# Optimization experiments

Hardware: AMD Instinct MI355X
Metric: run time of the kernel (lower is better)

Reference implementation:

```python
import jax, jax.numpy as jnp
import numpy as np

N = 20000      # atoms
E = 320000     # pairs (avg degree 16)
F = 64         # per-atom features
NRBF = 32      # radial basis functions
RC = 1.0       # maximum_interaction_radius


def _decompose(t):
    # X = I + A + S (irreducible decomposition of 3x3 tensors)
    diag_mean = jnp.diagonal(t, axis1=-2, axis2=-1).mean(-1)
    I = diag_mean[..., None, None] * jnp.eye(3, dtype=t.dtype)
    A = 0.5 * (t - jnp.swapaxes(t, -1, -2))
    S = 0.5 * (t + jnp.swapaxes(t, -1, -2)) - I
    return I, A, S


def _tnorm(t):
    # Frobenius norm^2 over the trailing 3x3 -> [N, F]
    return (t ** 2).sum((-2, -1))


def _lin_t(t, W):
    # channel-mixing linear on the feature axis of [N, F, 3, 3]
    return jnp.einsum('nfij,gf->ngij', t, W)


def setup_inputs():
    key = jax.random.key(0)
    ks = jax.random.split(key, 14)
    inp = {
        'X': jax.random.normal(ks[0], (N, F, 3, 3), jnp.float32) * 0.1,
        'pair_indices': jax.random.randint(ks[1], (2, E), 0, N, jnp.int32),
        'd_ij': jax.random.uniform(ks[2], (E, 1), jnp.float32),
        'radial_feature_vector': jax.random.normal(ks[3], (E, NRBF), jnp.float32),
        'atomic_charges': jax.random.normal(ks[4], (N,), jnp.float32) * 0.1,
        # mlp_scalar: NRBF -> F -> 2F -> 3F (Dense = Linear + activation)
        'W0': jax.random.normal(ks[5], (F, NRBF), jnp.float32) / np.sqrt(NRBF),
        'b0': jnp.zeros((F,), jnp.float32),
        'W1': jax.random.normal(ks[6], (2 * F, F), jnp.float32) / np.sqrt(F),
        'b1': jnp.zeros((2 * F,), jnp.float32),
        'W2': jax.random.normal(ks[7], (3 * F, 2 * F), jnp.float32) / np.sqrt(2 * F),
        'b2': jnp.zeros((3 * F,), jnp.float32),
        # 6 bias-free FxF tensor linears
        'Wt': jax.random.normal(ks[8], (6, F, F), jnp.float32) / np.sqrt(F),
    }
    return inp


def reference(X, pair_indices, d_ij, radial_feature_vector, atomic_charges,
              W0, b0, W1, b1, W2, b2, Wt):
    silu = jax.nn.silu
    n_atoms = X.shape[0]
    src = pair_indices[1]  # gathered
    dst = pair_indices[0]  # scattered (index_add_)

    # cosine cutoff, [E, 1]
    C = (0.5 * (jnp.cos(jnp.pi * d_ij / RC) + 1.0)
         * (d_ij < RC).astype(X.dtype)).reshape(-1, 1)

    h = silu(radial_feature_vector @ W0.T + b0)
    h = silu(h @ W1.T + b1)
    h = silu(h @ W2.T + b2)                 # [E, 3F]
    rfv = (h * C).reshape(-1, F, 3)          # [E, F, 3]

    X = X / (_tnorm(X) + 1.0)[..., None, None]
    I, A, S = _decompose(X)
    I = _lin_t(I, Wt[0])
    A = _lin_t(A, Wt[1])
    S = _lin_t(S, Wt[2])
    Y = I + A + S

    def mp(r, T):
        # gather-mul-scatter: [E,F,3,3] messages reduced to [N,F,3,3]
        msg = r[:, :, None, None] * T[src]
        return jax.ops.segment_sum(msg, dst, num_segments=n_atoms)

    msg = mp(rfv[..., 0], I) + mp(rfv[..., 1], A) + mp(rfv[..., 2], S)

    # O(3) group
    q = (1.0 + 0.1 * atomic_charges)[:, None, None, None]
    I, A, S = _decompose(q * (jnp.matmul(msg, Y) + jnp.matmul(Y, msg)))

    normp1 = (_tnorm(I + A + S) + 1.0)[..., None, None]
    I, A, S = I / normp1, A / normp1, S / normp1
    I = _lin_t(I, Wt[3])
    A = _lin_t(A, Wt[4])
    S = _lin_t(S, Wt[5])
    dX = I + A + S

    X = X + dX + q * jnp.matmul(dX, dX)
    return X
```

## Files before the change

kernel.cpp:

```cpp
#include <hip/hip_runtime.h>
#include <hip/hip_bf16.h>
#include <cmath>

#define N_ATOMS 20000
#define NE      320000
#define FDIM    64
#define NRBF    32
#define PI_F    3.14159265358979323846f

typedef __attribute__((ext_vector_type(8))) short bf16x8;
typedef __attribute__((ext_vector_type(4))) float f32x4;
typedef __attribute__((ext_vector_type(4))) _Float16 f16x4;

#define MFMA16(a, b, c) __builtin_amdgcn_mfma_f32_16x16x32_bf16(a, b, c, 0, 0, 0)

__device__ __forceinline__ float silu(float x) {
    return x * __builtin_amdgcn_rcpf(1.0f + __expf(-x));
}

__device__ __forceinline__ unsigned short f2bf_rne(float x) {
    unsigned u = __float_as_uint(x);
    u += 0x7fffu + ((u >> 16) & 1u);
    return (unsigned short)(u >> 16);
}

__device__ __forceinline__ void split8(const float* v, bf16x8& hi, bf16x8& lo) {
#pragma unroll
    for (int j = 0; j < 8; j++) {
        unsigned u = __float_as_uint(v[j]);
        float hf = __uint_as_float(u & 0xffff0000u);
        hi[j] = (short)(u >> 16);
        lo[j] = (short)f2bf_rne(v[j] - hf);
    }
}

__global__ void prep_kernel(const float* __restrict__ Wt, float* __restrict__ wtT,
                            const float* __restrict__ W0, const float* __restrict__ W1,
                            const float* __restrict__ W2,
                            unsigned short* __restrict__ f0h, unsigned short* __restrict__ f0l,
                            unsigned short* __restrict__ f1h, unsigned short* __restrict__ f1l,
                            unsigned short* __restrict__ f2h, unsigned short* __restrict__ f2l,
                            const int* __restrict__ dst, int* __restrict__ deg) {
    int idx = blockIdx.x * 256 + threadIdx.x;
    if (idx < 24576) {
        int k = idx >> 12;
        int r = idx & 4095;
        int g = r >> 6;
        int f = r & 63;
        wtT[k * 4096 + f * 64 + g] = Wt[idx];
    } else if (idx < 59392) {
        int t = idx - 24576;
        const float* W;
        unsigned short *fh, *fl;
        int K, NT;
        if (t < 2048)       { W = W0; fh = f0h; fl = f0l;             K = 32;  NT = 4; }
        else if (t < 10240) { W = W1; fh = f1h; fl = f1l; t -= 2048;  K = 64;  NT = 8; }
        else                { W = W2; fh = f2h; fl = f2l; t -= 10240; K = 128; NT = 12; }
        int j = t & 7;
        int lane = (t >> 3) & 63;
        int rest = t >> 9;
        int nt = rest % NT;
        int ks = rest / NT;
        int k = ks * 32 + ((lane >> 4) & 3) * 8 + j;
        int n = nt * 16 + (lane & 15);
        float w = W[n * K + k];
        unsigned u = __float_as_uint(w);
        float hf = __uint_as_float(u & 0xffff0000u);
        fh[t] = (unsigned short)(u >> 16);
        fl[t] = f2bf_rne(w - hf);
    } else if (idx < 59392 + NE) {
        int e = idx - 59392;
        atomicAdd(&deg[dst[e]], 1);
    }
}

__global__ void scan_kernel(const int* __restrict__ deg, int* __restrict__ off) {
    __shared__ int part[1024];
    int t = threadIdx.x;
    const int CH = (N_ATOMS + 1023) / 1024;
    int base = t * CH;
    int s = 0;
    for (int i = 0; i < CH; i++) {
        int idx = base + i;
        if (idx < N_ATOMS) s += deg[idx];
    }
    part[t] = s;
    __syncthreads();
    for (int ofs = 1; ofs < 1024; ofs <<= 1) {
        int v = (t >= ofs) ? part[t - ofs] : 0;
        __syncthreads();
        part[t] += v;
        __syncthreads();
    }
    int run = (t == 0) ? 0 : part[t - 1];
    for (int i = 0; i < CH; i++) {
        int idx = base + i;
        if (idx < N_ATOMS) {
            off[idx] = run;
            run += deg[idx];
        }
    }
    if (t == 1023) off[N_ATOMS] = run;
}

__global__ void fill_kernel(const int* __restrict__ dst, const int* __restrict__ srcArr,
                            const int* __restrict__ off, int* __restrict__ cursor,
                            int* __restrict__ sbkt, int* __restrict__ slotOf) {
    int e = blockIdx.x * 256 + threadIdx.x;
    if (e >= NE) return;
    int d = dst[e];
    int pos = atomicAdd(&cursor[d], 1);
    int slot = off[d] + pos;
    sbkt[slot] = srcArr[e];
    slotOf[e] = slot;
}

#define H1S 68
#define H2S 132
__global__ __launch_bounds__(128) void mlp_mfma_kernel(
    const float* __restrict__ rfv, const float* __restrict__ dij,
    const float* __restrict__ b0, const float* __restrict__ b1, const float* __restrict__ b2,
    const unsigned short* __restrict__ f0h, const unsigned short* __restrict__ f0l,
    const unsigned short* __restrict__ f1h, const unsigned short* __restrict__ f1l,
    const unsigned short* __restrict__ f2h, const unsigned short* __restrict__ f2l,
    const int* __restrict__ slotOf,
    __hip_bfloat16* __restrict__ r) {
    __shared__ float h1s[2][32][H1S];
    __shared__ float h2s[2][32][H2S];
    const int w = threadIdx.x >> 6;
    const int lane = threadIdx.x & 63;
    const int q = lane >> 4;
    const int c = lane & 15;
    const int e0 = (blockIdx.x * 2 + w) * 32;
    float (*h1)[H1S] = h1s[w];
    float (*h2)[H2S] = h2s[w];

    {
        bf16x8 ah[2], al[2];
#pragma unroll
        for (int mt = 0; mt < 2; mt++) {
            float v[8];
            const float* p = rfv + (size_t)(e0 + mt * 16 + c) * 32 + q * 8;
            *(float4*)(v)     = *(const float4*)(p);
            *(float4*)(v + 4) = *(const float4*)(p + 4);
            split8(v, ah[mt], al[mt]);
        }
#pragma unroll
        for (int nt = 0; nt < 4; nt++) {
            float bias = b0[nt * 16 + c];
            f32x4 acc[2];
            acc[0] = {bias, bias, bias, bias};
            acc[1] = acc[0];
            bf16x8 bh = *(const bf16x8*)(f0h + (size_t)(nt * 64 + lane) * 8);
            bf16x8 bl = *(const bf16x8*)(f0l + (size_t)(nt * 64 + lane) * 8);
#pragma unroll
            for (int mt = 0; mt < 2; mt++) {
                acc[mt] = MFMA16(al[mt], bh, acc[mt]);
                acc[mt] = MFMA16(ah[mt], bl, acc[mt]);
                acc[mt] = MFMA16(ah[mt], bh, acc[mt]);
            }
#pragma unroll
            for (int mt = 0; mt < 2; mt++)
#pragma unroll
                for (int reg = 0; reg < 4; reg++)
                    h1[mt * 16 + q * 4 + reg][nt * 16 + c] = silu(acc[mt][reg]);
        }
    }

    {
        bf16x8 ah[2][2], al[2][2];
#pragma unroll
        for (int mt = 0; mt < 2; mt++)
#pragma unroll
            for (int ks = 0; ks < 2; ks++) {
                float v[8];
                const float* p = &h1[mt * 16 + c][ks * 32 + q * 8];
                *(float4*)(v)     = *(const float4*)(p);
                *(float4*)(v + 4) = *(const float4*)(p + 4);
                split8(v, ah[mt][ks], al[mt][ks]);
            }
#pragma unroll
        for (int nt = 0; nt < 8; nt++) {
            float bias = b1[nt * 16 + c];
            f32x4 acc[2];
            acc[0] = {bias, bias, bias, bias};
            acc[1] = acc[0];
#pragma unroll
            for (int ks = 0; ks < 2; ks++) {
                bf16x8 bh = *(const bf16x8*)(f1h + (size_t)((ks * 8 + nt) * 64 + lane) * 8);
                bf16x8 bl = *(const bf16x8*)(f1l + (size_t)((ks * 8 + nt) * 64 + lane) * 8);
#pragma unroll
                for (int mt = 0; mt < 2; mt++) {
                    acc[mt] = MFMA16(al[mt][ks], bh, acc[mt]);
                    acc[mt] = MFMA16(ah[mt][ks], bl, acc[mt]);
                    acc[mt] = MFMA16(ah[mt][ks], bh, acc[mt]);
                }
            }
#pragma unroll
            for (int mt = 0; mt < 2; mt++)
#pragma unroll
                for (int reg = 0; reg < 4; reg++)
                    h2[mt * 16 + q * 4 + reg][nt * 16 + c] = silu(acc[mt][reg]);
        }
    }

    {
        bf16x8 ah[2][4], al[2][4];
#pragma unroll
        for (int mt = 0; mt < 2; mt++)
#pragma unroll
            for (int ks = 0; ks < 4; ks++) {
                float v[8];
                const float* p = &h2[mt * 16 + c][ks * 32 + q * 8];
                *(float4*)(v)     = *(const float4*)(p);
                *(float4*)(v + 4) = *(const float4*)(p + 4);
                split8(v, ah[mt][ks], al[mt][ks]);
            }
        float cut[2][4];
        int srow[2][4];
#pragma unroll
        for (int mt = 0; mt < 2; mt++)
#pragma unroll
            for (int reg = 0; reg < 4; reg++) {
                int e = e0 + mt * 16 + q * 4 + reg;
                float d = dij[e];
                cut[mt][reg] = (d < 1.0f) ? 0.5f * (__cosf(PI_F * d) + 1.0f) : 0.0f;
                srow[mt][reg] = slotOf[e];
            }
#pragma unroll
        for (int nt = 0; nt < 12; nt++) {
            float bias = b2[nt * 16 + c];
            f32x4 acc[2];
            acc[0] = {bias, bias, bias, bias};
            acc[1] = acc[0];
#pragma unroll
            for (int ks = 0; ks < 4; ks++) {
                bf16x8 bh = *(const bf16x8*)(f2h + (size_t)((ks * 12 + nt) * 64 + lane) * 8);
                bf16x8 bl = *(const bf16x8*)(f2l + (size_t)((ks * 12 + nt) * 64 + lane) * 8);
#pragma unroll
                for (int mt = 0; mt < 2; mt++) {
                    acc[mt] = MFMA16(al[mt][ks], bh, acc[mt]);
                    acc[mt] = MFMA16(ah[mt][ks], bl, acc[mt]);
                    acc[mt] = MFMA16(ah[mt][ks], bh, acc[mt]);
                }
            }
#pragma unroll
            for (int mt = 0; mt < 2; mt++)
#pragma unroll
                for (int reg = 0; reg < 4; reg++)
                    r[(size_t)srow[mt][reg] * 192 + nt * 16 + c] =
                        __float2bfloat16(silu(acc[mt][reg]) * cut[mt][reg]);
        }
    }
}

__global__ __launch_bounds__(256) void lin1_kernel(
    const float* __restrict__ X, const float* __restrict__ wtT,
    _Float16* __restrict__ comp, float* __restrict__ Yb) {
    __shared__ float lds[4][64 * 11];
    int w = threadIdx.x >> 6;
    int l = threadIdx.x & 63;
    int a = blockIdx.x * 4 + w;

    {
        const float* x = X + ((size_t)a * 64 + l) * 9;
        float v[9];
#pragma unroll
        for (int i = 0; i < 9; i++) v[i] = x[i];
        float t2 = 0.f;
#pragma unroll
        for (int i = 0; i < 9; i++) t2 += v[i] * v[i];
        float inv = 1.0f / (t2 + 1.0f);
#pragma unroll
        for (int i = 0; i < 9; i++) v[i] *= inv;
        float iso = (v[0] + v[4] + v[8]) * (1.0f / 3.0f);
        float* o = &lds[w][l * 11];
        o[0] = iso;
        o[1] = 0.5f * (v[1] - v[3]);
        o[2] = 0.5f * (v[2] - v[6]);
        o[3] = 0.5f * (v[5] - v[7]);
        o[4] = v[0] - iso;
        o[5] = 0.5f * (v[1] + v[3]);
        o[6] = 0.5f * (v[2] + v[6]);
        o[7] = v[4] - iso;
        o[8] = 0.5f * (v[5] + v[7]);
        o[9] = v[8] - iso;
    }
    __syncthreads();
    {
        int g = l;
        const float* w0 = wtT;
        const float* w1 = wtT + 4096;
        const float* w2 = wtT + 8192;
        float acc[10];
#pragma unroll
        for (int c = 0; c < 10; c++) acc[c] = 0.f;
        for (int f = 0; f < 64; f++) {
            float wI = w0[f * 64 + g];
            float wA = w1[f * 64 + g];
            float wS = w2[f * 64 + g];
            const float* rf = &lds[w][f * 11];
            acc[0] += wI * rf[0];
            acc[1] += wA * rf[1];
            acc[2] += wA * rf[2];
            acc[3] += wA * rf[3];
#pragma unroll
            for (int c = 4; c < 10; c++) acc[c] += wS * rf[c];
        }
        _Float16* co = comp + ((size_t)a * 64 + g) * 12;
        f16x4 c0 = {(_Float16)acc[0], (_Float16)acc[1], (_Float16)acc[2], (_Float16)acc[3]};
        f16x4 c1 = {(_Float16)acc[4], (_Float16)acc[5], (_Float16)acc[6], (_Float16)acc[7]};
        f16x4 c2 = {(_Float16)acc[8], (_Float16)acc[9], (_Float16)0.f, (_Float16)0.f};
        *(f16x4*)(co)     = c0;
        *(f16x4*)(co + 4) = c1;
        *(f16x4*)(co + 8) = c2;
        float* y = Yb + ((size_t)a * 64 + g) * 9;
        y[0] = acc[0] + acc[4];
        y[1] = acc[5] + acc[1];
        y[2] = acc[6] + acc[2];
        y[3] = acc[5] - acc[1];
        y[4] = acc[0] + acc[7];
        y[5] = acc[8] + acc[3];
        y[6] = acc[6] - acc[2];
        y[7] = acc[8] - acc[3];
        y[8] = acc[0] + acc[9];
    }
}

__global__ __launch_bounds__(256) void msg_lin2_kernel(
    const int* __restrict__ off, const int* __restrict__ sbkt,
    const __hip_bfloat16* __restrict__ r,
    const _Float16* __restrict__ comp, const float* __restrict__ Yb,
    const float* __restrict__ X, const float* __restrict__ charges,
    const float* __restrict__ wtT, float* __restrict__ out) {
    __shared__ float lds[4][64 * 11];
    int w = threadIdx.x >> 6;
    int l = threadIdx.x & 63;
    int a = blockIdx.x * 4 + w;
    float q = 1.0f + 0.1f * charges[a];

    float m[10];
#pragma unroll
    for (int c = 0; c < 10; c++) m[c] = 0.f;
    {
        int beg = off[a], end = off[a + 1];
        if (beg < end) {
            __hip_bfloat16 ra, rb, rc;
            f16x4 c0, c1, c2;
            {
                const __hip_bfloat16* rp = r + (size_t)beg * 192 + l * 3;
                ra = rp[0]; rb = rp[1]; rc = rp[2];
                const _Float16* cp = comp + ((size_t)sbkt[beg] * 64 + l) * 12;
                c0 = *(const f16x4*)(cp);
                c1 = *(const f16x4*)(cp + 4);
                c2 = *(const f16x4*)(cp + 8);
            }
            for (int i = beg + 1; i < end; i++) {
                const __hip_bfloat16* rp = r + (size_t)i * 192 + l * 3;
                __hip_bfloat16 na = rp[0], nb = rp[1], nc = rp[2];
                const _Float16* cp = comp + ((size_t)sbkt[i] * 64 + l) * 12;
                f16x4 n0 = *(const f16x4*)(cp);
                f16x4 n1 = *(const f16x4*)(cp + 4);
                f16x4 n2 = *(const f16x4*)(cp + 8);
                float r0 = __bfloat162float(ra);
                float r1 = __bfloat162float(rb);
                float r2 = __bfloat162float(rc);
                m[0] += r0 * (float)c0[0];
                m[1] += r1 * (float)c0[1];
                m[2] += r1 * (float)c0[2];
                m[3] += r1 * (float)c0[3];
                m[4] += r2 * (float)c1[0];
                m[5] += r2 * (float)c1[1];
                m[6] += r2 * (float)c1[2];
                m[7] += r2 * (float)c1[3];
                m[8] += r2 * (float)c2[0];
                m[9] += r2 * (float)c2[1];
                ra = na; rb = nb; rc = nc;
                c0 = n0; c1 = n1; c2 = n2;
            }
            float r0 = __bfloat162float(ra);
            float r1 = __bfloat162float(rb);
            float r2 = __bfloat162float(rc);
            m[0] += r0 * (float)c0[0];
            m[1] += r1 * (float)c0[1];
            m[2] += r1 * (float)c0[2];
            m[3] += r1 * (float)c0[3];
            m[4] += r2 * (float)c1[0];
            m[5] += r2 * (float)c1[1];
            m[6] += r2 * (float)c1[2];
            m[7] += r2 * (float)c1[3];
            m[8] += r2 * (float)c2[0];
            m[9] += r2 * (float)c2[1];
        }
    }

    {
        float M[9];
        M[0] = m[0] + m[4]; M[1] = m[5] + m[1]; M[2] = m[6] + m[2];
        M[3] = m[5] - m[1]; M[4] = m[0] + m[7]; M[5] = m[8] + m[3];
        M[6] = m[6] - m[2]; M[7] = m[8] - m[3]; M[8] = m[0] + m[9];
        const float* yp = Yb + ((size_t)a * 64 + l) * 9;
        float Y[9];
#pragma unroll
        for (int i = 0; i < 9; i++) Y[i] = yp[i];
        float P[9];
#pragma unroll
        for (int i = 0; i < 3; i++) {
#pragma unroll
            for (int j = 0; j < 3; j++) {
                float s = 0.f;
#pragma unroll
                for (int k = 0; k < 3; k++)
                    s += M[i * 3 + k] * Y[k * 3 + j] + Y[i * 3 + k] * M[k * 3 + j];
                P[i * 3 + j] = q * s;
            }
        }
        float t2 = 0.f;
#pragma unroll
        for (int i = 0; i < 9; i++) t2 += P[i] * P[i];
        float inv = 1.0f / (t2 + 1.0f);
        float iso = (P[0] + P[4] + P[8]) * (1.0f / 3.0f);
        float* o = &lds[w][l * 11];
        o[0] = iso * inv;
        o[1] = 0.5f * (P[1] - P[3]) * inv;
        o[2] = 0.5f * (P[2] - P[6]) * inv;
        o[3] = 0.5f * (P[5] - P[7]) * inv;
        o[4] = (P[0] - iso) * inv;
        o[5] = 0.5f * (P[1] + P[3]) * inv;
        o[6] = 0.5f * (P[2] + P[6]) * inv;
        o[7] = (P[4] - iso) * inv;
        o[8] = 0.5f * (P[5] + P[7]) * inv;
        o[9] = (P[8] - iso) * inv;
    }
    __syncthreads();
    {
        int g = l;
        const float* w3 = wtT + 3 * 4096;
        const float* w4 = wtT + 4 * 4096;
        const float* w5 = wtT + 5 * 4096;
        float acc[10];
#pragma unroll
        for (int c = 0; c < 10; c++) acc[c] = 0.f;
        for (int f = 0; f < 64; f++) {
            float wI = w3[f * 64 + g];
            float wA = w4[f * 64 + g];
            float wS = w5[f * 64 + g];
            const float* rf = &lds[w][f * 11];
            acc[0] += wI * rf[0];
            acc[1] += wA * rf[1];
            acc[2] += wA * rf[2];
            acc[3] += wA * rf[3];
#pragma unroll
            for (int c = 4; c < 10; c++) acc[c] += wS * rf[c];
        }
        float D[9];
        D[0] = acc[0] + acc[4]; D[1] = acc[5] + acc[1]; D[2] = acc[6] + acc[2];
        D[3] = acc[5] - acc[1]; D[4] = acc[0] + acc[7]; D[5] = acc[8] + acc[3];
        D[6] = acc[6] - acc[2]; D[7] = acc[8] - acc[3]; D[8] = acc[0] + acc[9];

        const float* x = X + ((size_t)a * 64 + g) * 9;
        float xv[9];
#pragma unroll
        for (int i = 0; i < 9; i++) xv[i] = x[i];
        float t2 = 0.f;
#pragma unroll
        for (int i = 0; i < 9; i++) t2 += xv[i] * xv[i];
        float invn = 1.0f / (t2 + 1.0f);
#pragma unroll
        for (int i = 0; i < 9; i++) xv[i] *= invn;

        float DD[9];
#pragma unroll
        for (int i = 0; i < 3; i++) {
#pragma unroll
            for (int j = 0; j < 3; j++) {
                float s = 0.f;
#pragma unroll
                for (int k = 0; k < 3; k++) s += D[i * 3 + k] * D[k * 3 + j];
                DD[i * 3 + j] = s;
            }
        }
        float* op = out + ((size_t)a * 64 + g) * 9;
#pragma unroll
        for (int i = 0; i < 9; i++) op[i] = xv[i] + D[i] + q * DD[i];
    }
}

extern "C" void kernel_launch(void* const* d_in, const int* in_sizes, int n_in,
                              void* d_out, int out_size, void* d_ws, size_t ws_size,
                              hipStream_t stream) {
    const float* X       = (const float*)d_in[0];
    const int*   pair    = (const int*)d_in[1];
    const float* dij     = (const float*)d_in[2];
    const float* rfv     = (const float*)d_in[3];
    const float* charges = (const float*)d_in[4];
    const float* W0      = (const float*)d_in[5];
    const float* b0      = (const float*)d_in[6];
    const float* W1      = (const float*)d_in[7];
    const float* b1      = (const float*)d_in[8];
    const float* W2      = (const float*)d_in[9];
    const float* b2      = (const float*)d_in[10];
    const float* Wt      = (const float*)d_in[11];
    float* out = (float*)d_out;

    const int* dst = pair;
    const int* src = pair + NE;

    char* ws = (char*)d_ws;
    size_t ofs = 0;
    auto alloc = [&](size_t bytes) {
        void* p = ws + ofs;
        ofs += (bytes + 255) & ~(size_t)255;
        return p;
    };
    float* wtT  = (float*)alloc((size_t)6 * 4096 * 4);
    unsigned short* f0h = (unsigned short*)alloc(2048 * 2);
    unsigned short* f0l = (unsigned short*)alloc(2048 * 2);
    unsigned short* f1h = (unsigned short*)alloc(8192 * 2);
    unsigned short* f1l = (unsigned short*)alloc(8192 * 2);
    unsigned short* f2h = (unsigned short*)alloc(24576 * 2);
    unsigned short* f2l = (unsigned short*)alloc(24576 * 2);
    _Float16* comp = (_Float16*)alloc((size_t)N_ATOMS * FDIM * 12 * 2);
    __hip_bfloat16* rbuf = (__hip_bfloat16*)alloc((size_t)NE * 192 * 2);
    int* deg    = (int*)alloc((size_t)N_ATOMS * 4);
    int* offarr = (int*)alloc((size_t)(N_ATOMS + 1) * 4);
    int* cursor = (int*)alloc((size_t)N_ATOMS * 4);
    int* sbkt   = (int*)alloc((size_t)NE * 4);
    int* slotOf = (int*)alloc((size_t)NE * 4);
    float* Yb   = out;

    hipMemsetAsync(deg, 0, (size_t)N_ATOMS * 4, stream);
    hipMemsetAsync(cursor, 0, (size_t)N_ATOMS * 4, stream);

    prep_kernel<<<(59392 + NE + 255) / 256, 256, 0, stream>>>(
        Wt, wtT, W0, W1, W2, f0h, f0l, f1h, f1l, f2h, f2l, dst, deg);
    scan_kernel<<<1, 1024, 0, stream>>>(deg, offarr);
    fill_kernel<<<NE / 256, 256, 0, stream>>>(dst, src, offarr, cursor, sbkt, slotOf);

    mlp_mfma_kernel<<<NE / 64, 128, 0, stream>>>(
        rfv, dij, b0, b1, b2, f0h, f0l, f1h, f1l, f2h, f2l, slotOf, rbuf);

    lin1_kernel<<<N_ATOMS / 4, 256, 0, stream>>>(X, wtT, comp, Yb);

    msg_lin2_kernel<<<N_ATOMS / 4, 256, 0, stream>>>(
        offarr, sbkt, rbuf, comp, Yb, X, charges, wtT, out);
}
```

Baseline: 460.2 us.

## Fuse lin1 into MLP kernel and store radial weights in planar layout

```diff
diff --git a/kernel.cpp b/kernel.cpp
--- a/kernel.cpp
+++ b/kernel.cpp
@@ -117,14 +117,15 @@
 
 #define H1S 68
 #define H2S 132
-__global__ __launch_bounds__(128) void mlp_mfma_kernel(
+__global__ __launch_bounds__(128) void mlp_lin1_kernel(
     const float* __restrict__ rfv, const float* __restrict__ dij,
     const float* __restrict__ b0, const float* __restrict__ b1, const float* __restrict__ b2,
     const unsigned short* __restrict__ f0h, const unsigned short* __restrict__ f0l,
     const unsigned short* __restrict__ f1h, const unsigned short* __restrict__ f1l,
     const unsigned short* __restrict__ f2h, const unsigned short* __restrict__ f2l,
-    const int* __restrict__ slotOf,
-    __hip_bfloat16* __restrict__ r) {
+    const int* __restrict__ slotOf, __hip_bfloat16* __restrict__ r,
+    const float* __restrict__ X, const float* __restrict__ wtT,
+    _Float16* __restrict__ comp, float* __restrict__ Yb) {
     __shared__ float h1s[2][32][H1S];
     __shared__ float h2s[2][32][H2S];
     const int w = threadIdx.x >> 6;
@@ -244,86 +245,88 @@
                     acc[mt] = MFMA16(ah[mt][ks], bh, acc[mt]);
                 }
             }
+            int k = nt * 16 + c;
+            int ld = k / 3;
+            int jm = k - ld * 3;
+            int co = jm * 64 + ld;
 #pragma unroll
             for (int mt = 0; mt < 2; mt++)
 #pragma unroll
                 for (int reg = 0; reg < 4; reg++)
-                    r[(size_t)srow[mt][reg] * 192 + nt * 16 + c] =
+                    r[(size_t)srow[mt][reg] * 192 + co] =
                         __float2bfloat16(silu(acc[mt][reg]) * cut[mt][reg]);
         }
     }
-}
-
-__global__ __launch_bounds__(256) void lin1_kernel(
-    const float* __restrict__ X, const float* __restrict__ wtT,
-    _Float16* __restrict__ comp, float* __restrict__ Yb) {
-    __shared__ float lds[4][64 * 11];
-    int w = threadIdx.x >> 6;
-    int l = threadIdx.x & 63;
-    int a = blockIdx.x * 4 + w;
-
-    {
-        const float* x = X + ((size_t)a * 64 + l) * 9;
-        float v[9];
-#pragma unroll
-        for (int i = 0; i < 9; i++) v[i] = x[i];
-        float t2 = 0.f;
-#pragma unroll
-        for (int i = 0; i < 9; i++) t2 += v[i] * v[i];
-        float inv = 1.0f / (t2 + 1.0f);
-#pragma unroll
-        for (int i = 0; i < 9; i++) v[i] *= inv;
-        float iso = (v[0] + v[4] + v[8]) * (1.0f / 3.0f);
-        float* o = &lds[w][l * 11];
-        o[0] = iso;
-        o[1] = 0.5f * (v[1] - v[3]);
-        o[2] = 0.5f * (v[2] - v[6]);
-        o[3] = 0.5f * (v[5] - v[7]);
-        o[4] = v[0] - iso;
-        o[5] = 0.5f * (v[1] + v[3]);
-        o[6] = 0.5f * (v[2] + v[6]);
-        o[7] = v[4] - iso;
-        o[8] = 0.5f * (v[5] + v[7]);
-        o[9] = v[8] - iso;
-    }
-    __syncthreads();
-    {
-        int g = l;
-        const float* w0 = wtT;
-        const float* w1 = wtT + 4096;
-        const float* w2 = wtT + 8192;
-        float acc[10];
-#pragma unroll
-        for (int c = 0; c < 10; c++) acc[c] = 0.f;
-        for (int f = 0; f < 64; f++) {
-            float wI = w0[f * 64 + g];
-            float wA = w1[f * 64 + g];
-            float wS = w2[f * 64 + g];
-            const float* rf = &lds[w][f * 11];
-            acc[0] += wI * rf[0];
-            acc[1] += wA * rf[1];
-            acc[2] += wA * rf[2];
-            acc[3] += wA * rf[3];
-#pragma unroll
-            for (int c = 4; c < 10; c++) acc[c] += wS * rf[c];
-        }
-        _Float16* co = comp + ((size_t)a * 64 + g) * 12;
-        f16x4 c0 = {(_Float16)acc[0], (_Float16)acc[1], (_Float16)acc[2], (_Float16)acc[3]};
-        f16x4 c1 = {(_Float16)acc[4], (_Float16)acc[5], (_Float16)acc[6], (_Float16)acc[7]};
-        f16x4 c2 = {(_Float16)acc[8], (_Float16)acc[9], (_Float16)0.f, (_Float16)0.f};
-        *(f16x4*)(co)     = c0;
-        *(f16x4*)(co + 4) = c1;
-        *(f16x4*)(co + 8) = c2;
-        float* y = Yb + ((size_t)a * 64 + g) * 9;
-        y[0] = acc[0] + acc[4];
-        y[1] = acc[5] + acc[1];
-        y[2] = acc[6] + acc[2];
-        y[3] = acc[5] - acc[1];
-        y[4] = acc[0] + acc[7];
-        y[5] = acc[8] + acc[3];
-        y[6] = acc[6] - acc[2];
-        y[7] = acc[8] - acc[3];
-        y[8] = acc[0] + acc[9];
+
+    {
+        float* stg = &h1s[w][0][0];
+#pragma unroll
+        for (int at = 0; at < 2; at++) {
+            int a = blockIdx.x * 4 + w * 2 + at;
+            int l = lane;
+            {
+                const float* x = X + ((size_t)a * 64 + l) * 9;
+                float v[9];
+#pragma unroll
+                for (int i = 0; i < 9; i++) v[i] = x[i];
+                float t2 = 0.f;
+#pragma unroll
+                for (int i = 0; i < 9; i++) t2 += v[i] * v[i];
+                float inv = 1.0f / (t2 + 1.0f);
+#pragma unroll
+                for (int i = 0; i < 9; i++) v[i] *= inv;
+                float iso = (v[0] + v[4] + v[8]) * (1.0f / 3.0f);
+                float* o = &stg[l * 11];
+                o[0] = iso;
+                o[1] = 0.5f * (v[1] - v[3]);
+                o[2] = 0.5f * (v[2] - v[6]);
+                o[3] = 0.5f * (v[5] - v[7]);
+                o[4] = v[0] - iso;
+                o[5] = 0.5f * (v[1] + v[3]);
+                o[6] = 0.5f * (v[2] + v[6]);
+                o[7] = v[4] - iso;
+                o[8] = 0.5f * (v[5] + v[7]);
+                o[9] = v[8] - iso;
+            }
+            {
+                int g = l;
+                const float* w0 = wtT;
+                const float* w1 = wtT + 4096;
+                const float* w2 = wtT + 8192;
+                float acc[10];
+#pragma unroll
+                for (int cc = 0; cc < 10; cc++) acc[cc] = 0.f;
+                for (int f = 0; f < 64; f++) {
+                    float wI = w0[f * 64 + g];
+                    float wA = w1[f * 64 + g];
+                    float wS = w2[f * 64 + g];
+                    const float* rf = &stg[f * 11];
+                    acc[0] += wI * rf[0];
+                    acc[1] += wA * rf[1];
+                    acc[2] += wA * rf[2];
+                    acc[3] += wA * rf[3];
+#pragma unroll
+                    for (int cc = 4; cc < 10; cc++) acc[cc] += wS * rf[cc];
+                }
+                _Float16* co = comp + ((size_t)a * 64 + g) * 12;
+                f16x4 c0 = {(_Float16)acc[0], (_Float16)acc[1], (_Float16)acc[2], (_Float16)acc[3]};
+                f16x4 c1 = {(_Float16)acc[4], (_Float16)acc[5], (_Float16)acc[6], (_Float16)acc[7]};
+                f16x4 c2 = {(_Float16)acc[8], (_Float16)acc[9], (_Float16)0.f, (_Float16)0.f};
+                *(f16x4*)(co)     = c0;
+                *(f16x4*)(co + 4) = c1;
+                *(f16x4*)(co + 8) = c2;
+                float* y = Yb + ((size_t)a * 64 + g) * 9;
+                y[0] = acc[0] + acc[4];
+                y[1] = acc[5] + acc[1];
+                y[2] = acc[6] + acc[2];
+                y[3] = acc[5] - acc[1];
+                y[4] = acc[0] + acc[7];
+                y[5] = acc[8] + acc[3];
+                y[6] = acc[6] - acc[2];
+                y[7] = acc[8] - acc[3];
+                y[8] = acc[0] + acc[9];
+            }
+        }
     }
 }
 
@@ -348,16 +351,16 @@
             __hip_bfloat16 ra, rb, rc;
             f16x4 c0, c1, c2;
             {
-                const __hip_bfloat16* rp = r + (size_t)beg * 192 + l * 3;
-                ra = rp[0]; rb = rp[1]; rc = rp[2];
+                const __hip_bfloat16* rp = r + (size_t)beg * 192 + l;
+                ra = rp[0]; rb = rp[64]; rc = rp[128];
                 const _Float16* cp = comp + ((size_t)sbkt[beg] * 64 + l) * 12;
                 c0 = *(const f16x4*)(cp);
                 c1 = *(const f16x4*)(cp + 4);
                 c2 = *(const f16x4*)(cp + 8);
             }
             for (int i = beg + 1; i < end; i++) {
-                const __hip_bfloat16* rp = r + (size_t)i * 192 + l * 3;
-                __hip_bfloat16 na = rp[0], nb = rp[1], nc = rp[2];
+                const __hip_bfloat16* rp = r + (size_t)i * 192 + l;
+                __hip_bfloat16 na = rp[0], nb = rp[64], nc = rp[128];
                 const _Float16* cp = comp + ((size_t)sbkt[i] * 64 + l) * 12;
                 f16x4 n0 = *(const f16x4*)(cp);
                 f16x4 n1 = *(const f16x4*)(cp + 4);
@@ -537,10 +540,9 @@
     scan_kernel<<<1, 1024, 0, stream>>>(deg, offarr);
     fill_kernel<<<NE / 256, 256, 0, stream>>>(dst, src, offarr, cursor, sbkt, slotOf);
 
-    mlp_mfma_kernel<<<NE / 64, 128, 0, stream>>>(
-        rfv, dij, b0, b1, b2, f0h, f0l, f1h, f1l, f2h, f2l, slotOf, rbuf);
-
-    lin1_kernel<<<N_ATOMS / 4, 256, 0, stream>>>(X, wtT, comp, Yb);
+    mlp_lin1_kernel<<<NE / 64, 128, 0, stream>>>(
+        rfv, dij, b0, b1, b2, f0h, f0l, f1h, f1l, f2h, f2l, slotOf, rbuf,
+        X, wtT, comp, Yb);
 
     msg_lin2_kernel<<<N_ATOMS / 4, 256, 0, stream>>>(
         offarr, sbkt, rbuf, comp, Yb, X, charges, wtT, out);
```

New measurement: 549.8 us. 1.19x slower.
